# Kernel tuning notes

Hardware: AMD Instinct MI355X
Metric: run time of the kernel (lower is better)

## Reference

```python
import jax, jax.numpy as jnp
import numpy as np

N_NODES = 100000
N_EDGES = 1600000
F_IN, H1, H2, N_CLS = 512, 180, 120, 40
NEG_SLOPE = 0.01  # F.leaky_relu default


def setup_inputs() -> dict:
    key = jax.random.key(0)
    ks = jax.random.split(key, 8)
    x = jax.random.normal(ks[0], (N_NODES, F_IN), dtype=jnp.float32)
    edge_index = jax.random.randint(ks[1], (2, N_EDGES), 0, N_NODES, dtype=jnp.int64)
    W1 = jax.random.normal(ks[2], (F_IN, H1), dtype=jnp.float32) / np.sqrt(F_IN)
    b1 = jnp.zeros((H1,), dtype=jnp.float32)
    W2 = jax.random.normal(ks[3], (H1, H2), dtype=jnp.float32) / np.sqrt(H1)
    b2 = jnp.zeros((H2,), dtype=jnp.float32)
    W3 = jax.random.normal(ks[4], (H2, N_CLS), dtype=jnp.float32) / np.sqrt(H2)
    b3 = jnp.zeros((N_CLS,), dtype=jnp.float32)
    return {"x": x, "edge_index": edge_index, "W1": W1, "b1": b1,
            "W2": W2, "b2": b2, "W3": W3, "b3": b3}


def _add_self_loops(edge_index, n):
    loop = jnp.arange(n, dtype=edge_index.dtype)
    src = jnp.concatenate([edge_index[0], loop])
    dst = jnp.concatenate([edge_index[1], loop])
    return src, dst


def _gcn_conv(h, src, dst, norm, W, b, n):
    # PyG GCNConv: linear transform first, then normalized scatter-add at dst.
    h = h @ W  # [N, out]
    msg = norm[:, None] * h[src]  # gather at source, per-edge scale
    out = jax.ops.segment_sum(msg, dst, num_segments=n)  # scatter-add at dest
    return out + b


def reference(x, edge_index, W1, b1, W2, b2, W3, b3):
    n = x.shape[0]
    src, dst = _add_self_loops(edge_index, n)
    # symmetric normalization deg^-1/2 * deg^-1/2 on self-loop-augmented graph
    ones = jnp.ones(dst.shape[0], dtype=x.dtype)
    deg = jax.ops.segment_sum(ones, dst, num_segments=n)
    dinv = jnp.where(deg > 0, jax.lax.rsqrt(deg), 0.0)
    norm = dinv[src] * dinv[dst]  # [E+N]

    h = _gcn_conv(x, src, dst, norm, W1, b1, n)
    h = jnp.where(h >= 0, h, NEG_SLOPE * h)
    h = _gcn_conv(h, src, dst, norm, W2, b2, n)
    h = jnp.where(h >= 0, h, NEG_SLOPE * h)
    logits = h @ W3 + b3
    return jax.nn.log_softmax(logits, axis=1)
```

## Files before the change

kernel.cpp:

```cpp
#include <hip/hip_runtime.h>
#include <math.h>

typedef __attribute__((ext_vector_type(8))) short short8;
typedef __attribute__((ext_vector_type(4))) float f32x4;

static constexpr int F_IN = 512;
static constexpr int H1V = 180, H1P = 192;
static constexpr int H2V = 120, H2P = 128;
static constexpr int NC  = 40,  NCP = 64;

__device__ inline unsigned f2bf(float f) {
    unsigned u = __float_as_uint(f);
    return (u + 0x7fffu + ((u >> 16) & 1u)) >> 16;
}
__device__ inline unsigned cvtpk(float lo, float hi) {
    unsigned r;
    asm("v_cvt_pk_bf16_f32 %0, %1, %2" : "=v"(r) : "v"(lo), "v"(hi));
    return r;
}
#define BLO(u) __uint_as_float((u) << 16)
#define BHI(u) __uint_as_float((u) & 0xffff0000u)

__device__ inline void gload_lds16(const void* gsrc, void* ldst) {
    __builtin_amdgcn_global_load_lds(
        (const __attribute__((address_space(1))) void*)gsrc,
        (__attribute__((address_space(3))) void*)ldst, 16, 0, 0);
}

__global__ void k_init(const int* __restrict__ ei, int* __restrict__ flag,
                       const float* __restrict__ W1, const float* __restrict__ W2,
                       const float* __restrict__ W3, const float* __restrict__ b1,
                       const float* __restrict__ b2, const float* __restrict__ b3,
                       unsigned short* __restrict__ W1s, unsigned short* __restrict__ W2s,
                       unsigned short* __restrict__ W3s, float* __restrict__ b1p,
                       float* __restrict__ b2p, float* __restrict__ b3p) {
    if (blockIdx.x < 16) {
        int i = blockIdx.x * 256 + threadIdx.x;
        if (ei[2 * i + 1] != 0) flag[0] = 1;
        return;
    }
    const int n1 = F_IN * H1P;
    const int n2 = n1 + H1P * H2P;
    const int n3 = n2 + H2P * NCP;
    const int n4 = n3 + H1P;
    const int n5 = n4 + H2P;
    const int n6 = n5 + NCP;
    int i = (blockIdx.x - 16) * 256 + threadIdx.x;
    if (i < n1) {
        int k = i / H1P, c = i % H1P;
        float v = (c < H1V) ? W1[k * H1V + c] : 0.0f;
        W1s[(size_t)(k >> 3) * H1P * 8 + c * 8 + (k & 7)] = (unsigned short)f2bf(v);
    } else if (i < n2) {
        int j = i - n1;
        int k = j / H2P, c = j % H2P;
        float v = (k < H1V && c < H2V) ? W2[k * H2V + c] : 0.0f;
        W2s[(size_t)(k >> 3) * H2P * 8 + c * 8 + (k & 7)] = (unsigned short)f2bf(v);
    } else if (i < n3) {
        int j = i - n2;
        int k = j / NCP, c = j % NCP;
        float v = (k < H2V && c < NC) ? W3[k * NC + c] : 0.0f;
        W3s[(size_t)(k >> 3) * NCP * 8 + c * 8 + (k & 7)] = (unsigned short)f2bf(v);
    } else if (i < n4) {
        int c = i - n3;
        b1p[c] = (c < H1V) ? b1[c] : 0.0f;
    } else if (i < n5) {
        int c = i - n4;
        b2p[c] = (c < H2V) ? b2[c] : 0.0f;
    } else if (i < n6) {
        int c = i - n5;
        b3p[c] = (c < NC) ? b3[c] : -1e30f;
    }
}

__global__ void k_hist(const int* __restrict__ ei, int E, const int* __restrict__ flag,
                       int* __restrict__ deg, int* __restrict__ rank) {
    int e = blockIdx.x * 256 + threadIdx.x;
    if (e >= E) return;
    bool i64 = (flag[0] == 0);
    int d = i64 ? ei[2 * E + 2 * e] : ei[E + e];
    rank[e] = atomicAdd(&deg[d], 1);
}

__global__ void k_scan1(const int* __restrict__ deg, int* __restrict__ rp,
                        int* __restrict__ bsum, float* __restrict__ dinv, int n) {
    __shared__ int s[256];
    int t = threadIdx.x;
    int base = blockIdx.x * 1024 + t * 4;
    int v0 = (base + 0 < n) ? deg[base + 0] : 0;
    int v1 = (base + 1 < n) ? deg[base + 1] : 0;
    int v2 = (base + 2 < n) ? deg[base + 2] : 0;
    int v3 = (base + 3 < n) ? deg[base + 3] : 0;
    if (base + 0 < n) dinv[base + 0] = rsqrtf((float)(v0 + 1));
    if (base + 1 < n) dinv[base + 1] = rsqrtf((float)(v1 + 1));
    if (base + 2 < n) dinv[base + 2] = rsqrtf((float)(v2 + 1));
    if (base + 3 < n) dinv[base + 3] = rsqrtf((float)(v3 + 1));
    int sum = v0 + v1 + v2 + v3;
    s[t] = sum;
    __syncthreads();
    for (int off = 1; off < 256; off <<= 1) {
        int x = (t >= off) ? s[t - off] : 0;
        __syncthreads();
        s[t] += x;
        __syncthreads();
    }
    int run = s[t] - sum;
    if (t == 255) bsum[blockIdx.x] = s[255];
    if (base + 0 < n) rp[base + 0] = run; run += v0;
    if (base + 1 < n) rp[base + 1] = run; run += v1;
    if (base + 2 < n) rp[base + 2] = run; run += v2;
    if (base + 3 < n) rp[base + 3] = run;
}

__global__ void k_scan2(int* __restrict__ bsum, int nb) {
    __shared__ int s[128];
    int t = threadIdx.x;
    int v = (t < nb) ? bsum[t] : 0;
    s[t] = v;
    __syncthreads();
    for (int off = 1; off < 128; off <<= 1) {
        int x = (t >= off) ? s[t - off] : 0;
        __syncthreads();
        s[t] += x;
        __syncthreads();
    }
    if (t < nb) bsum[t] = s[t] - v;
}

__global__ void k_scan3(const int* __restrict__ bsum, int* __restrict__ rp,
                        int n, int E) {
    int i = blockIdx.x * 256 + threadIdx.x;
    if (i < n) {
        rp[i] = rp[i] + bsum[i >> 10];
    } else if (i == n) {
        rp[n] = E;
    }
}

__global__ __launch_bounds__(256) void k_fill(const int* __restrict__ ei, int E,
                                              const int* __restrict__ flag,
                                              const int* __restrict__ rp,
                                              const int* __restrict__ rank,
                                              int* __restrict__ csr,
                                              int bw, int chunk) {
    int bkt = blockIdx.x & 7;
    int lo = bkt * bw, hi = lo + bw;
    int ch = blockIdx.x >> 3;
    int e0 = ch * chunk;
    int e1 = min(E, e0 + chunk);
    bool i64 = (flag[0] == 0);
    for (int e = e0 + (int)threadIdx.x; e < e1; e += 256) {
        int d = i64 ? ei[2 * E + 2 * e] : ei[E + e];
        if (d >= lo && d < hi) {
            int s = i64 ? ei[2 * e] : ei[e];
            csr[rp[d] + rank[e]] = s;
        }
    }
}

__global__ __launch_bounds__(512) void k_gemm1(const float* __restrict__ X,
                                               const short8* __restrict__ Bs,
                                               const float* __restrict__ dinv,
                                               signed char* __restrict__ Hq,
                                               float* __restrict__ sc,
                                               int M) {
    __shared__ float ldsf[8192];
    char* lds = (char*)ldsf;
    int t = threadIdx.x;
    int w = t >> 6, l = t & 63;
    int lr = l & 15, kg = l >> 4;
    int wr = w >> 2, wc = w & 3;
    int row0 = blockIdx.x * 128;
    int colb = wc * 48;

    f32x4 acc[4][3];
#pragma unroll
    for (int m = 0; m < 4; ++m)
#pragma unroll
        for (int nn = 0; nn < 3; ++nn) acc[m][nn] = (f32x4){0.f, 0.f, 0.f, 0.f};

    auto stage = [&](int kb, int buf) {
#pragma unroll
        for (int j = 0; j < 2; ++j) {
            int o = j * 8192 + t * 16;
            int row = o >> 7;
            int col4 = ((o >> 4) & 7) ^ (row & 7);
            int rowg = row0 + row;
            if (rowg >= M) rowg = M - 1;
            gload_lds16(X + (size_t)rowg * F_IN + kb + col4 * 4,
                        lds + buf * 16384 + j * 8192 + w * 1024);
        }
    };

    stage(0, 0);
    __syncthreads();

    for (int ts = 0; ts < 16; ++ts) {
        int cur = ts & 1;
        if (ts < 15) stage((ts + 1) * 32, cur ^ 1);
        short8 b[3];
#pragma unroll
        for (int nn = 0; nn < 3; ++nn)
            b[nn] = Bs[(size_t)(ts * 4 + kg) * H1P + colb + nn * 16 + lr];
        short8 a[4];
#pragma unroll
        for (int m = 0; m < 4; ++m) {
            int row = wr * 64 + m * 16 + lr;
            char* base = lds + cur * 16384 + row * 128;
            float4 v0 = *(const float4*)(base + (((2 * kg + 0) ^ (row & 7)) * 16));
            float4 v1 = *(const float4*)(base + (((2 * kg + 1) ^ (row & 7)) * 16));
            union { unsigned u[4]; short8 s; } cu;
            cu.u[0] = cvtpk(v0.x, v0.y);
            cu.u[1] = cvtpk(v0.z, v0.w);
            cu.u[2] = cvtpk(v1.x, v1.y);
            cu.u[3] = cvtpk(v1.z, v1.w);
            a[m] = cu.s;
        }
#pragma unroll
        for (int m = 0; m < 4; ++m)
#pragma unroll
            for (int nn = 0; nn < 3; ++nn)
                acc[m][nn] = __builtin_amdgcn_mfma_f32_16x16x32_bf16(a[m], b[nn], acc[m][nn], 0, 0, 0);
        __syncthreads();
    }

    float* rmaxp = (float*)lds;
#pragma unroll
    for (int m = 0; m < 4; ++m) {
#pragma unroll
        for (int j = 0; j < 4; ++j) {
            int rl = wr * 64 + m * 16 + kg * 4 + j;
            int grow = row0 + rl;
            float dv = (grow < M) ? dinv[grow] : 0.f;
            float lm = 0.f;
#pragma unroll
            for (int nn = 0; nn < 3; ++nn)
                lm = fmaxf(lm, fabsf(acc[m][nn][j] * dv));
#pragma unroll
            for (int d = 1; d < 16; d <<= 1)
                lm = fmaxf(lm, __shfl_xor(lm, d));
            if (lr == 0) rmaxp[rl * 4 + wc] = lm;
        }
    }
    __syncthreads();
#pragma unroll
    for (int m = 0; m < 4; ++m) {
#pragma unroll
        for (int j = 0; j < 4; ++j) {
            int rl = wr * 64 + m * 16 + kg * 4 + j;
            int grow = row0 + rl;
            if (grow >= M) continue;
            float dv = dinv[grow];
            float rm = fmaxf(fmaxf(rmaxp[rl * 4 + 0], rmaxp[rl * 4 + 1]),
                             fmaxf(rmaxp[rl * 4 + 2], rmaxp[rl * 4 + 3]));
            float inv = (rm > 0.f) ? 127.0f / rm : 0.f;
            if (wc == 0 && lr == 0) sc[grow] = rm * (1.0f / 127.0f);
#pragma unroll
            for (int nn = 0; nn < 3; ++nn) {
                float v = acc[m][nn][j] * dv * inv;
                v = fminf(fmaxf(rintf(v), -127.f), 127.f);
                Hq[(size_t)grow * H1P + colb + nn * 16 + lr] = (signed char)(int)v;
            }
        }
    }
}

__global__ __launch_bounds__(256) void k_gat1q(const signed char* __restrict__ Hq,
                                               const float* __restrict__ sc,
                                               const float* __restrict__ dinv,
                                               const int* __restrict__ rp,
                                               const int* __restrict__ csr,
                                               const float* __restrict__ bias,
                                               uint2* __restrict__ out, int n) {
    int wv = threadIdx.x >> 6, l = threadIdx.x & 63;
    int i = blockIdx.x * 4 + wv;
    if (i >= n) return;
    bool act = l < 48;
    int c = act ? l : 0;
    const unsigned* Hr = (const unsigned*)(Hq + c * 4);

    float a0, a1, a2, a3;
    {
        unsigned w0 = Hr[(size_t)i * 48];
        float s0 = sc[i];
        a0 = (float)(signed char)(w0) * s0;
        a1 = (float)(signed char)(w0 >> 8) * s0;
        a2 = (float)(signed char)(w0 >> 16) * s0;
        a3 = (float)(signed char)(w0 >> 24) * s0;
    }
    float p0 = 0.f, p1 = 0.f, p2 = 0.f, p3 = 0.f;

    int e0 = rp[i], e1 = rp[i + 1];
    int e = e0;
    for (; e + 7 < e1; e += 8) {
        int s[8];
#pragma unroll
        for (int q = 0; q < 8; ++q) s[q] = csr[e + q];
        float scs[8];
#pragma unroll
        for (int q = 0; q < 8; ++q) scs[q] = sc[s[q]];
        unsigned v[8];
#pragma unroll
        for (int q = 0; q < 8; ++q) v[q] = Hr[(size_t)s[q] * 48];
#pragma unroll
        for (int q = 0; q < 8; q += 2) {
            a0 = fmaf((float)(signed char)(v[q]), scs[q], a0);
            a1 = fmaf((float)(signed char)(v[q] >> 8), scs[q], a1);
            a2 = fmaf((float)(signed char)(v[q] >> 16), scs[q], a2);
            a3 = fmaf((float)(signed char)(v[q] >> 24), scs[q], a3);
            p0 = fmaf((float)(signed char)(v[q + 1]), scs[q + 1], p0);
            p1 = fmaf((float)(signed char)(v[q + 1] >> 8), scs[q + 1], p1);
            p2 = fmaf((float)(signed char)(v[q + 1] >> 16), scs[q + 1], p2);
            p3 = fmaf((float)(signed char)(v[q + 1] >> 24), scs[q + 1], p3);
        }
    }
    for (; e < e1; ++e) {
        int s0 = csr[e];
        float sq = sc[s0];
        unsigned w0 = Hr[(size_t)s0 * 48];
        a0 = fmaf((float)(signed char)(w0), sq, a0);
        a1 = fmaf((float)(signed char)(w0 >> 8), sq, a1);
        a2 = fmaf((float)(signed char)(w0 >> 16), sq, a2);
        a3 = fmaf((float)(signed char)(w0 >> 24), sq, a3);
    }
    a0 += p0; a1 += p1; a2 += p2; a3 += p3;

    float di = dinv[i];
    float4 bb = *(const float4*)(bias + 4 * c);
    float o0 = fmaf(di, a0, bb.x);
    float o1 = fmaf(di, a1, bb.y);
    float o2 = fmaf(di, a2, bb.z);
    float o3 = fmaf(di, a3, bb.w);
    o0 = o0 >= 0.f ? o0 : 0.01f * o0;
    o1 = o1 >= 0.f ? o1 : 0.01f * o1;
    o2 = o2 >= 0.f ? o2 : 0.01f * o2;
    o3 = o3 >= 0.f ? o3 : 0.01f * o3;
    if (act) {
        uint2 r;
        r.x = (f2bf(o1) << 16) | f2bf(o0);
        r.y = (f2bf(o3) << 16) | f2bf(o2);
        out[(size_t)i * 48 + c] = r;
    }
}

__global__ __launch_bounds__(512) void k_gemm2(const unsigned short* __restrict__ A,
                                               const short8* __restrict__ Bs,
                                               const float* __restrict__ dinv,
                                               unsigned short* __restrict__ Hout,
                                               int M) {
    __shared__ unsigned short ldsu[16384];
    char* lds = (char*)ldsu;
    int t = threadIdx.x;
    int w = t >> 6, l = t & 63;
    int lr = l & 15, kg = l >> 4;
    int wr = w >> 2, wc = w & 3;
    int row0 = blockIdx.x * 128;
    int colb = wc * 32;

    f32x4 acc[4][2];
#pragma unroll
    for (int m = 0; m < 4; ++m)
#pragma unroll
        for (int nn = 0; nn < 2; ++nn) acc[m][nn] = (f32x4){0.f, 0.f, 0.f, 0.f};

    auto stage = [&](int kb, int buf) {
#pragma unroll
        for (int j = 0; j < 2; ++j) {
            int o = j * 8192 + t * 16;
            int row = o >> 7;
            int chunk = ((o >> 4) & 7) ^ (row & 7);
            int rowg = row0 + row;
            if (rowg >= M) rowg = M - 1;
            gload_lds16(A + (size_t)rowg * H1P + kb + chunk * 8,
                        lds + buf * 16384 + j * 8192 + w * 1024);
        }
    };

    stage(0, 0);
    __syncthreads();

    for (int ts = 0; ts < 3; ++ts) {
        int cur = ts & 1;
        if (ts < 2) stage((ts + 1) * 64, cur ^ 1);
        short8 b[2][2];
#pragma unroll
        for (int kk = 0; kk < 2; ++kk)
#pragma unroll
            for (int nn = 0; nn < 2; ++nn)
                b[kk][nn] = Bs[(size_t)(ts * 8 + kk * 4 + kg) * H2P + colb + nn * 16 + lr];
        short8 a[2][4];
#pragma unroll
        for (int kk = 0; kk < 2; ++kk)
#pragma unroll
            for (int m = 0; m < 4; ++m) {
                int row = wr * 64 + m * 16 + lr;
                a[kk][m] = *(const short8*)(lds + cur * 16384 + row * 128 +
                                            (((kk * 4 + kg) ^ (row & 7)) * 16));
            }
#pragma unroll
        for (int kk = 0; kk < 2; ++kk)
#pragma unroll
            for (int m = 0; m < 4; ++m)
#pragma unroll
                for (int nn = 0; nn < 2; ++nn)
                    acc[m][nn] = __builtin_amdgcn_mfma_f32_16x16x32_bf16(a[kk][m], b[kk][nn], acc[m][nn], 0, 0, 0);
        __syncthreads();
    }

#pragma unroll
    for (int m = 0; m < 4; ++m) {
        int r4 = row0 + wr * 64 + m * 16 + kg * 4;
#pragma unroll
        for (int j = 0; j < 4; ++j) {
            int grow = r4 + j;
            if (grow < M) {
                float dv = dinv[grow];
#pragma unroll
                for (int nn = 0; nn < 2; ++nn)
                    Hout[(size_t)grow * H2P + colb + nn * 16 + lr] =
                        (unsigned short)f2bf(acc[m][nn][j] * dv);
            }
        }
    }
}

__global__ __launch_bounds__(256) void k_gat2(const uint2* __restrict__ H,
                                              const float* __restrict__ dinv,
                                              const int* __restrict__ rp,
                                              const int* __restrict__ csr,
                                              const float* __restrict__ bias,
                                              uint2* __restrict__ out, int n) {
    int wv = threadIdx.x >> 6, l = threadIdx.x & 63;
    int half = l >> 5, c = l & 31;
    int i = blockIdx.x * 8 + wv * 2 + half;
    if (i >= n) return;
    const uint2* Hr = H + c;

    float a0, a1, a2, a3;
    {
        uint2 v = Hr[(size_t)i * 32];
        a0 = BLO(v.x); a1 = BHI(v.x); a2 = BLO(v.y); a3 = BHI(v.y);
    }
    float p0 = 0.f, p1 = 0.f, p2 = 0.f, p3 = 0.f;

    int e0 = rp[i], e1 = rp[i + 1];
    int e = e0;
    for (; e + 7 < e1; e += 8) {
        int s[8];
#pragma unroll
        for (int q = 0; q < 8; ++q) s[q] = csr[e + q];
        uint2 v[8];
#pragma unroll
        for (int q = 0; q < 8; ++q) v[q] = Hr[(size_t)s[q] * 32];
#pragma unroll
        for (int q = 0; q < 8; q += 2) {
            a0 += BLO(v[q].x); a1 += BHI(v[q].x); a2 += BLO(v[q].y); a3 += BHI(v[q].y);
            p0 += BLO(v[q + 1].x); p1 += BHI(v[q + 1].x); p2 += BLO(v[q + 1].y); p3 += BHI(v[q + 1].y);
        }
    }
    for (; e + 3 < e1; e += 4) {
        int s0 = csr[e], s1 = csr[e + 1], s2 = csr[e + 2], s3 = csr[e + 3];
        uint2 va = Hr[(size_t)s0 * 32];
        uint2 vb = Hr[(size_t)s1 * 32];
        uint2 vc = Hr[(size_t)s2 * 32];
        uint2 vd = Hr[(size_t)s3 * 32];
        a0 += BLO(va.x); a1 += BHI(va.x); a2 += BLO(va.y); a3 += BHI(va.y);
        p0 += BLO(vb.x); p1 += BHI(vb.x); p2 += BLO(vb.y); p3 += BHI(vb.y);
        a0 += BLO(vc.x); a1 += BHI(vc.x); a2 += BLO(vc.y); a3 += BHI(vc.y);
        p0 += BLO(vd.x); p1 += BHI(vd.x); p2 += BLO(vd.y); p3 += BHI(vd.y);
    }
    for (; e < e1; ++e) {
        int s0 = csr[e];
        uint2 va = Hr[(size_t)s0 * 32];
        a0 += BLO(va.x); a1 += BHI(va.x); a2 += BLO(va.y); a3 += BHI(va.y);
    }
    a0 += p0; a1 += p1; a2 += p2; a3 += p3;

    float di = dinv[i];
    float4 bb = *(const float4*)(bias + 4 * c);
    float o0 = fmaf(di, a0, bb.x);
    float o1 = fmaf(di, a1, bb.y);
    float o2 = fmaf(di, a2, bb.z);
    float o3 = fmaf(di, a3, bb.w);
    o0 = o0 >= 0.f ? o0 : 0.01f * o0;
    o1 = o1 >= 0.f ? o1 : 0.01f * o1;
    o2 = o2 >= 0.f ? o2 : 0.01f * o2;
    o3 = o3 >= 0.f ? o3 : 0.01f * o3;
    uint2 r;
    r.x = (f2bf(o1) << 16) | f2bf(o0);
    r.y = (f2bf(o3) << 16) | f2bf(o2);
    out[(size_t)i * 32 + c] = r;
}

__global__ __launch_bounds__(256) void k_out(const unsigned short* __restrict__ H,
                                             const short8* __restrict__ Bs,
                                             const float* __restrict__ b3p,
                                             float* __restrict__ out, int M) {
    int t = threadIdx.x;
    int w = t >> 6, l = t & 63;
    int lr = l & 15, kg = l >> 4;
    int row0 = blockIdx.x * 64 + w * 16;

    f32x4 acc[4];
#pragma unroll
    for (int f = 0; f < 4; ++f) acc[f] = (f32x4){0.f, 0.f, 0.f, 0.f};

    int rowa = row0 + lr;
    if (rowa >= M) rowa = M - 1;
    const unsigned short* arow = H + (size_t)rowa * H2P;

#pragma unroll
    for (int ks = 0; ks < 4; ++ks) {
        short8 a = *(const short8*)(arow + ks * 32 + kg * 8);
#pragma unroll
        for (int f = 0; f < 4; ++f) {
            short8 b = Bs[(size_t)(ks * 4 + kg) * NCP + f * 16 + lr];
            acc[f] = __builtin_amdgcn_mfma_f32_16x16x32_bf16(a, b, acc[f], 0, 0, 0);
        }
    }

    float bl[4];
#pragma unroll
    for (int f = 0; f < 4; ++f) bl[f] = b3p[f * 16 + lr];

#pragma unroll
    for (int j = 0; j < 4; ++j) {
        int grow = row0 + kg * 4 + j;
        float lg[4];
#pragma unroll
        for (int f = 0; f < 4; ++f) lg[f] = acc[f][j] + bl[f];
        float m = fmaxf(fmaxf(lg[0], lg[1]), fmaxf(lg[2], lg[3]));
#pragma unroll
        for (int d = 1; d < 16; d <<= 1) m = fmaxf(m, __shfl_xor(m, d));
        float s = expf(lg[0] - m) + expf(lg[1] - m) + expf(lg[2] - m) + expf(lg[3] - m);
#pragma unroll
        for (int d = 1; d < 16; d <<= 1) s += __shfl_xor(s, d);
        float lse = m + logf(s);
        if (grow < M) {
#pragma unroll
            for (int f = 0; f < 4; ++f) {
                int c = f * 16 + lr;
                if (c < NC) out[(size_t)grow * NC + c] = lg[f] - lse;
            }
        }
    }
}

extern "C" void kernel_launch(void* const* d_in, const int* in_sizes, int n_in,
                              void* d_out, int out_size, void* d_ws, size_t ws_size,
                              hipStream_t stream) {
    const float* x  = (const float*)d_in[0];
    const int*   ei = (const int*)d_in[1];
    const float* W1 = (const float*)d_in[2];
    const float* b1 = (const float*)d_in[3];
    const float* W2 = (const float*)d_in[4];
    const float* b2 = (const float*)d_in[5];
    const float* W3 = (const float*)d_in[6];
    const float* b3 = (const float*)d_in[7];
    float* outp = (float*)d_out;

    int n = in_sizes[0] / F_IN;
    int E = in_sizes[1] / 2;

    char* p = (char*)d_ws;
    auto alloc = [&](size_t bytes) -> char* {
        char* r = p;
        p += (bytes + 511) & ~(size_t)511;
        return r;
    };
    int*            fd     = (int*)alloc((size_t)(n + 1) * 4);
    int*            flag   = fd;
    int*            deg    = fd + 1;
    float*          dinv   = (float*)alloc((size_t)n * 4);
    int*            rp     = (int*)alloc((size_t)(n + 1) * 4);
    int*            bsum   = (int*)alloc(4096);
    int*            rank   = (int*)alloc((size_t)E * 4);
    int*            csr    = (int*)alloc((size_t)E * 4);
    unsigned short* W1s    = (unsigned short*)alloc((size_t)F_IN * H1P * 2);
    unsigned short* W2s    = (unsigned short*)alloc((size_t)H1P * H2P * 2);
    unsigned short* W3s    = (unsigned short*)alloc((size_t)H2P * NCP * 2);
    float*          b1p    = (float*)alloc(H1P * 4);
    float*          b2p    = (float*)alloc(H2P * 4);
    float*          b3p    = (float*)alloc(NCP * 4);
    signed char*    h1q    = (signed char*)alloc((size_t)n * H1P);
    float*          sc     = (float*)alloc((size_t)n * 4);
    unsigned short* h1agg  = (unsigned short*)alloc((size_t)n * H1P * 2);
    unsigned short* h2     = (unsigned short*)alloc((size_t)n * H2P * 2);
    unsigned short* h2agg  = (unsigned short*)alloc((size_t)n * H2P * 2);

    hipMemsetAsync(fd, 0, (size_t)(n + 1) * 4, stream);

    k_init<<<530, 256, 0, stream>>>(ei, flag, W1, W2, W3, b1, b2, b3,
                                    W1s, W2s, W3s, b1p, b2p, b3p);

    int eb = (E + 255) / 256;
    k_hist<<<eb, 256, 0, stream>>>(ei, E, flag, deg, rank);

    int nb = (n + 1023) / 1024;
    k_scan1<<<nb, 256, 0, stream>>>(deg, rp, bsum, dinv, n);
    k_scan2<<<1, 128, 0, stream>>>(bsum, nb);
    k_scan3<<<(n + 1 + 255) / 256, 256, 0, stream>>>(bsum, rp, n, E);

    int bw = (n + 7) / 8;
    int nch = 256;
    int chunk = (E + nch - 1) / nch;
    k_fill<<<nch * 8, 256, 0, stream>>>(ei, E, flag, rp, rank, csr, bw, chunk);

    int gb = (n + 127) / 128;
    k_gemm1<<<gb, 512, 0, stream>>>(x, (const short8*)W1s, dinv, h1q, sc, n);
    k_gat1q<<<(n + 3) / 4, 256, 0, stream>>>(h1q, sc, dinv, rp, csr, b1p,
                                             (uint2*)h1agg, n);
    k_gemm2<<<gb, 512, 0, stream>>>(h1agg, (const short8*)W2s, dinv, h2, n);
    k_gat2<<<(n + 7) / 8, 256, 0, stream>>>((const uint2*)h2, dinv, rp, csr, b2p,
                                            (uint2*)h2agg, n);
    k_out<<<(n + 63) / 64, 256, 0, stream>>>(h2agg, (const short8*)W3s, b3p, outp, n);
}
```

Measured before the change: 373.1 us.

## Compact edge arrays for CSR fill and retile first GEMM to 64 rows

The histogram kernel now writes compact dst and (src, rank) arrays. The CSR fill pass reads these instead of re-reading the strided int64 edge_index, which it does eight times (once per bucket). The first GEMM goes from 128-row blocks with 8 waves to 64-row blocks with 4 waves, and each staged K slice doubles to 64 columns. That halves the number of barriers and doubles the block count. The cost is extra workspace writes (12 bytes per edge) in the histogram kernel and less reuse of W1 loads per block.

```diff
diff --git a/kernel.cpp b/kernel.cpp
--- a/kernel.cpp
+++ b/kernel.cpp
@@ -73,12 +73,17 @@
 }
 
 __global__ void k_hist(const int* __restrict__ ei, int E, const int* __restrict__ flag,
-                       int* __restrict__ deg, int* __restrict__ rank) {
+                       int* __restrict__ deg, int* __restrict__ dst32,
+                       uint2* __restrict__ sr) {
     int e = blockIdx.x * 256 + threadIdx.x;
     if (e >= E) return;
     bool i64 = (flag[0] == 0);
-    int d = i64 ? ei[2 * E + 2 * e] : ei[E + e];
-    rank[e] = atomicAdd(&deg[d], 1);
+    int s, d;
+    if (i64) { s = ei[2 * e]; d = ei[2 * E + 2 * e]; }
+    else     { s = ei[e];     d = ei[E + e]; }
+    int r = atomicAdd(&deg[d], 1);
+    dst32[e] = d;
+    sr[e] = make_uint2((unsigned)s, (unsigned)r);
 }
 
 __global__ void k_scan1(const int* __restrict__ deg, int* __restrict__ rp,
@@ -136,10 +141,9 @@
     }
 }
 
-__global__ __launch_bounds__(256) void k_fill(const int* __restrict__ ei, int E,
-                                              const int* __restrict__ flag,
+__global__ __launch_bounds__(256) void k_fill(const int* __restrict__ dst32,
+                                              const uint2* __restrict__ sr, int E,
                                               const int* __restrict__ rp,
-                                              const int* __restrict__ rank,
                                               int* __restrict__ csr,
                                               int bw, int chunk) {
     int bkt = blockIdx.x & 7;
@@ -147,17 +151,16 @@
     int ch = blockIdx.x >> 3;
     int e0 = ch * chunk;
     int e1 = min(E, e0 + chunk);
-    bool i64 = (flag[0] == 0);
     for (int e = e0 + (int)threadIdx.x; e < e1; e += 256) {
-        int d = i64 ? ei[2 * E + 2 * e] : ei[E + e];
+        int d = dst32[e];
         if (d >= lo && d < hi) {
-            int s = i64 ? ei[2 * e] : ei[e];
-            csr[rp[d] + rank[e]] = s;
-        }
-    }
-}
-
-__global__ __launch_bounds__(512) void k_gemm1(const float* __restrict__ X,
+            uint2 v = sr[e];
+            csr[rp[d] + (int)v.y] = (int)v.x;
+        }
+    }
+}
+
+__global__ __launch_bounds__(256) void k_gemm1(const float* __restrict__ X,
                                                const short8* __restrict__ Bs,
                                                const float* __restrict__ dinv,
                                                signed char* __restrict__ Hq,
@@ -168,9 +171,8 @@
     int t = threadIdx.x;
     int w = t >> 6, l = t & 63;
     int lr = l & 15, kg = l >> 4;
-    int wr = w >> 2, wc = w & 3;
-    int row0 = blockIdx.x * 128;
-    int colb = wc * 48;
+    int row0 = blockIdx.x * 64;
+    int colb = w * 48;
 
     f32x4 acc[4][3];
 #pragma unroll
@@ -180,46 +182,50 @@
 
     auto stage = [&](int kb, int buf) {
 #pragma unroll
-        for (int j = 0; j < 2; ++j) {
-            int o = j * 8192 + t * 16;
-            int row = o >> 7;
-            int col4 = ((o >> 4) & 7) ^ (row & 7);
+        for (int j = 0; j < 4; ++j) {
+            int o = j * 4096 + t * 16;
+            int row = o >> 8;
+            int col4 = ((o >> 4) & 15) ^ (row & 15);
             int rowg = row0 + row;
             if (rowg >= M) rowg = M - 1;
             gload_lds16(X + (size_t)rowg * F_IN + kb + col4 * 4,
-                        lds + buf * 16384 + j * 8192 + w * 1024);
+                        lds + buf * 16384 + j * 4096 + w * 1024);
         }
     };
 
     stage(0, 0);
     __syncthreads();
 
-    for (int ts = 0; ts < 16; ++ts) {
+    for (int ts = 0; ts < 8; ++ts) {
         int cur = ts & 1;
-        if (ts < 15) stage((ts + 1) * 32, cur ^ 1);
-        short8 b[3];
-#pragma unroll
-        for (int nn = 0; nn < 3; ++nn)
-            b[nn] = Bs[(size_t)(ts * 4 + kg) * H1P + colb + nn * 16 + lr];
-        short8 a[4];
-#pragma unroll
-        for (int m = 0; m < 4; ++m) {
-            int row = wr * 64 + m * 16 + lr;
-            char* base = lds + cur * 16384 + row * 128;
-            float4 v0 = *(const float4*)(base + (((2 * kg + 0) ^ (row & 7)) * 16));
-            float4 v1 = *(const float4*)(base + (((2 * kg + 1) ^ (row & 7)) * 16));
-            union { unsigned u[4]; short8 s; } cu;
-            cu.u[0] = cvtpk(v0.x, v0.y);
-            cu.u[1] = cvtpk(v0.z, v0.w);
-            cu.u[2] = cvtpk(v1.x, v1.y);
-            cu.u[3] = cvtpk(v1.z, v1.w);
-            a[m] = cu.s;
-        }
-#pragma unroll
-        for (int m = 0; m < 4; ++m)
+        if (ts < 7) stage((ts + 1) * 64, cur ^ 1);
+#pragma unroll
+        for (int kk = 0; kk < 2; ++kk) {
+            short8 b[3];
 #pragma unroll
             for (int nn = 0; nn < 3; ++nn)
-                acc[m][nn] = __builtin_amdgcn_mfma_f32_16x16x32_bf16(a[m], b[nn], acc[m][nn], 0, 0, 0);
+                b[nn] = Bs[(size_t)(ts * 8 + kk * 4 + kg) * H1P + colb + nn * 16 + lr];
+            short8 a[4];
+#pragma unroll
+            for (int m = 0; m < 4; ++m) {
+                int row = m * 16 + lr;
+                char* base = lds + cur * 16384 + row * 256;
+                int c0 = kk * 8 + kg * 2;
+                float4 v0 = *(const float4*)(base + (((c0 + 0) ^ (row & 15)) * 16));
+                float4 v1 = *(const float4*)(base + (((c0 + 1) ^ (row & 15)) * 16));
+                union { unsigned u[4]; short8 s; } cu;
+                cu.u[0] = cvtpk(v0.x, v0.y);
+                cu.u[1] = cvtpk(v0.z, v0.w);
+                cu.u[2] = cvtpk(v1.x, v1.y);
+                cu.u[3] = cvtpk(v1.z, v1.w);
+                a[m] = cu.s;
+            }
+#pragma unroll
+            for (int m = 0; m < 4; ++m)
+#pragma unroll
+                for (int nn = 0; nn < 3; ++nn)
+                    acc[m][nn] = __builtin_amdgcn_mfma_f32_16x16x32_bf16(a[m], b[nn], acc[m][nn], 0, 0, 0);
+        }
         __syncthreads();
     }
 
@@ -228,7 +234,7 @@
     for (int m = 0; m < 4; ++m) {
 #pragma unroll
         for (int j = 0; j < 4; ++j) {
-            int rl = wr * 64 + m * 16 + kg * 4 + j;
+            int rl = m * 16 + kg * 4 + j;
             int grow = row0 + rl;
             float dv = (grow < M) ? dinv[grow] : 0.f;
             float lm = 0.f;
@@ -238,7 +244,7 @@
 #pragma unroll
             for (int d = 1; d < 16; d <<= 1)
                 lm = fmaxf(lm, __shfl_xor(lm, d));
-            if (lr == 0) rmaxp[rl * 4 + wc] = lm;
+            if (lr == 0) rmaxp[rl * 4 + w] = lm;
         }
     }
     __syncthreads();
@@ -246,14 +252,14 @@
     for (int m = 0; m < 4; ++m) {
 #pragma unroll
         for (int j = 0; j < 4; ++j) {
-            int rl = wr * 64 + m * 16 + kg * 4 + j;
+            int rl = m * 16 + kg * 4 + j;
             int grow = row0 + rl;
             if (grow >= M) continue;
             float dv = dinv[grow];
             float rm = fmaxf(fmaxf(rmaxp[rl * 4 + 0], rmaxp[rl * 4 + 1]),
                              fmaxf(rmaxp[rl * 4 + 2], rmaxp[rl * 4 + 3]));
             float inv = (rm > 0.f) ? 127.0f / rm : 0.f;
-            if (wc == 0 && lr == 0) sc[grow] = rm * (1.0f / 127.0f);
+            if (w == 0 && lr == 0) sc[grow] = rm * (1.0f / 127.0f);
 #pragma unroll
             for (int nn = 0; nn < 3; ++nn) {
                 float v = acc[m][nn][j] * dv * inv;
@@ -573,7 +579,8 @@
     float*          dinv   = (float*)alloc((size_t)n * 4);
     int*            rp     = (int*)alloc((size_t)(n + 1) * 4);
     int*            bsum   = (int*)alloc(4096);
-    int*            rank   = (int*)alloc((size_t)E * 4);
+    int*            dst32  = (int*)alloc((size_t)E * 4);
+    uint2*          sr     = (uint2*)alloc((size_t)E * 8);
     int*            csr    = (int*)alloc((size_t)E * 4);
     unsigned short* W1s    = (unsigned short*)alloc((size_t)F_IN * H1P * 2);
     unsigned short* W2s    = (unsigned short*)alloc((size_t)H1P * H2P * 2);
@@ -593,7 +600,7 @@
                                     W1s, W2s, W3s, b1p, b2p, b3p);
 
     int eb = (E + 255) / 256;
-    k_hist<<<eb, 256, 0, stream>>>(ei, E, flag, deg, rank);
+    k_hist<<<eb, 256, 0, stream>>>(ei, E, flag, deg, dst32, sr);
 
     int nb = (n + 1023) / 1024;
     k_scan1<<<nb, 256, 0, stream>>>(deg, rp, bsum, dinv, n);
@@ -603,13 +610,12 @@
     int bw = (n + 7) / 8;
     int nch = 256;
     int chunk = (E + nch - 1) / nch;
-    k_fill<<<nch * 8, 256, 0, stream>>>(ei, E, flag, rp, rank, csr, bw, chunk);
-
-    int gb = (n + 127) / 128;
-    k_gemm1<<<gb, 512, 0, stream>>>(x, (const short8*)W1s, dinv, h1q, sc, n);
+    k_fill<<<nch * 8, 256, 0, stream>>>(dst32, sr, E, rp, csr, bw, chunk);
+
+    k_gemm1<<<(n + 63) / 64, 256, 0, stream>>>(x, (const short8*)W1s, dinv, h1q, sc, n);
     k_gat1q<<<(n + 3) / 4, 256, 0, stream>>>(h1q, sc, dinv, rp, csr, b1p,
                                              (uint2*)h1agg, n);
-    k_gemm2<<<gb, 512, 0, stream>>>(h1agg, (const short8*)W2s, dinv, h2, n);
+    k_gemm2<<<(n + 127) / 128, 512, 0, stream>>>(h1agg, (const short8*)W2s, dinv, h2, n);
     k_gat2<<<(n + 7) / 8, 256, 0, stream>>>((const uint2*)h2, dinv, rp, csr, b2p,
                                             (uint2*)h2agg, n);
     k_out<<<(n + 63) / 64, 256, 0, stream>>>(h2agg, (const short8*)W3s, b3p, outp, n);
```

New measurement: 368.1 us. No clear change (-1.3%).
